# Kernel optimization log

Hardware: AMD Instinct MI355X
Metric: run time of the kernel (lower is better)

Reference implementation:

```python
import jax, jax.numpy as jnp
import numpy as np

TOKENS = 512
DIM_HEAD = 64
MAX_TOKENS = 2000
HEADS = 8
BATCH = 8


def _build_indices(tokens: int, max_tokens: int) -> np.ndarray:
    # Faithful replication of the torch index construction (done once in numpy).
    idx = np.arange(-tokens, tokens + 1)
    pad = max_tokens - 2 * tokens + 1
    row = np.concatenate([np.full(pad, idx[0]), idx, np.full(pad, idx[-1])])
    mat = np.stack([np.roll(row, i) for i in range(max_tokens)])
    mat = mat[: max_tokens - tokens + 2, max_tokens - tokens + 1 :]
    # torch fancy indexing wraps negative indices -> take mod of table size
    return (mat % (2 * tokens - 1)).astype(np.int32)


def setup_inputs() -> dict:
    key = jax.random.key(0)
    kq, kp = jax.random.split(key)
    scale = DIM_HEAD ** (-0.5)
    q = jax.random.normal(kq, (BATCH, HEADS, TOKENS, DIM_HEAD), dtype=jnp.float32)
    rel_pos_emb = (
        jax.random.normal(kp, (HEADS, 2 * TOKENS - 1, DIM_HEAD), dtype=jnp.float32)
        * scale
    )
    indices = jnp.asarray(_build_indices(TOKENS, MAX_TOKENS))
    return {"q": q, "rel_pos_emb": rel_pos_emb, "indices": indices}


def reference(q, rel_pos_emb, indices):
    t = q.shape[2]
    idx = indices[:t, :t]  # [r, t]
    # gather: [heads, r, t, dim_head]
    gathered = rel_pos_emb[:, idx]
    # emb[b,h,t,r] = sum_d q[b,h,t,d] * gathered[h,r,t,d]
    return jnp.einsum("bhtd,hrtd->bhtr", q, gathered)
```

## Files before the change

### kernel.cpp

```cpp
#include <hip/hip_runtime.h>
#include <hip/hip_bf16.h>


#define TOKENS 512
#define DIMH 64
#define NREL 1023
#define IDXN 1490

#define ESTR 72
#define PSTR 84

typedef short bf16x8 __attribute__((ext_vector_type(8)));
typedef float f32x4 __attribute__((ext_vector_type(4)));

__device__ __forceinline__ ushort4 cvt4(float4 v) {
    union { __hip_bfloat162 h2[2]; ushort4 s; } u;
    u.h2[0] = __float22bfloat162_rn(float2{v.x, v.y});
    u.h2[1] = __float22bfloat162_rn(float2{v.z, v.w});
    return u.s;
}
__device__ __forceinline__ bf16x8 cvt8(float4 a, float4 b) {
    union { __hip_bfloat162 h2[4]; bf16x8 v; } u;
    u.h2[0] = __float22bfloat162_rn(float2{a.x, a.y});
    u.h2[1] = __float22bfloat162_rn(float2{a.z, a.w});
    u.h2[2] = __float22bfloat162_rn(float2{b.x, b.y});
    u.h2[3] = __float22bfloat162_rn(float2{b.z, b.w});
    return u.v;
}

__global__ __launch_bounds__(256, 4)
void relpos_batch(const float* __restrict__ q,
                  const float* __restrict__ emb,
                  const int* __restrict__ indices,
                  float* __restrict__ out)
{
    __shared__ unsigned short Es[128 * ESTR];
    __shared__ float Ps[4 * 16 * PSTR];

    const int tid = threadIdx.x;
    const int blk = blockIdx.x;
    const int rt = blk & 7;
    const int tt = (blk >> 3) & 7;
    const int h  = (blk >> 6) & 7;
    const int bg = blk >> 9;
    const int t0 = tt * 64;
    const int r0 = rt * 64;

    const int j_a = indices[(size_t)(r0 + 63) * IDXN + t0];

    const int lane = tid & 63;
    const int wave = tid >> 6;
    const int quad = lane >> 4;
    const int l15  = lane & 15;

    {
        const float* embh = emb + (size_t)h * NREL * DIMH;
        const int c16 = tid & 15;
        const int rbase = tid >> 4;
#pragma unroll
        for (int it = 0; it < 8; ++it) {
            const int row = rbase + it * 16;
            int j = j_a + row;
            if (j >= NREL) j -= NREL;
            const float4 v = *(const float4*)(embh + (size_t)j * DIMH + c16 * 4);
            *(ushort4*)(Es + (size_t)row * ESTR + c16 * 4) = cvt4(v);
        }
    }

    const size_t qstep = (size_t)8 * TOKENS * DIMH;
    const float* qp = q + ((size_t)(bg * 32 + h) * TOKENS + t0 + wave * 16 + l15) * DIMH
                    + quad * 8;
    float4 qa0 = *(const float4*)qp;
    float4 qa1 = *(const float4*)(qp + 4);
    float4 qa2 = *(const float4*)(qp + 32);
    float4 qa3 = *(const float4*)(qp + 36);

    __syncthreads();

    bf16x8 ae[5][2];
#pragma unroll
    for (int i = 0; i < 5; ++i) {
        const unsigned short* bp = Es + (size_t)(wave * 16 + i * 16 + l15) * ESTR
                                 + quad * 8;
        ae[i][0] = *(const bf16x8*)bp;
        ae[i][1] = *(const bf16x8*)(bp + 32);
    }

    float* psw = Ps + (size_t)wave * 16 * PSTR;
    float* outw = out + ((size_t)(bg * 32 + h) * TOKENS + t0 + wave * 16) * (size_t)TOKENS
                + r0 + l15 * 4;

#pragma unroll
    for (int bi = 0; bi < 4; ++bi) {
        float4 nb0 = qa0, nb1 = qa1, nb2 = qa2, nb3 = qa3;
        if (bi < 3) {
            const float* np = qp + qstep * (bi + 1);
            nb0 = *(const float4*)np;
            nb1 = *(const float4*)(np + 4);
            nb2 = *(const float4*)(np + 32);
            nb3 = *(const float4*)(np + 36);
        }

        const bf16x8 bq0 = cvt8(qa0, qa1);
        const bf16x8 bq1 = cvt8(qa2, qa3);

#pragma unroll
        for (int i = 0; i < 5; ++i) {
            f32x4 acc = {0.f, 0.f, 0.f, 0.f};
            acc = __builtin_amdgcn_mfma_f32_16x16x32_bf16(ae[i][0], bq0, acc, 0, 0, 0);
            acc = __builtin_amdgcn_mfma_f32_16x16x32_bf16(ae[i][1], bq1, acc, 0, 0, 0);
            *(f32x4*)(psw + (size_t)l15 * PSTR + i * 16 + quad * 4) = acc;
        }

        float* ob = outw + (size_t)bi * 8 * TOKENS * TOKENS;
#pragma unroll
        for (int p = 0; p < 4; ++p) {
            const int u = quad + p * 4;
            const float* pr = psw + (size_t)u * PSTR + (u + 63 - l15 * 4);
            float4 o;
            o.x = pr[0];
            o.y = pr[-1];
            o.z = pr[-2];
            o.w = pr[-3];
            *(float4*)(ob + (size_t)u * TOKENS) = o;
        }

        qa0 = nb0; qa1 = nb1; qa2 = nb2; qa3 = nb3;
    }
}

extern "C" void kernel_launch(void* const* d_in, const int* in_sizes, int n_in,
                              void* d_out, int out_size, void* d_ws, size_t ws_size,
                              hipStream_t stream) {
    const float* q       = (const float*)d_in[0];
    const float* emb     = (const float*)d_in[1];
    const int*   indices = (const int*)d_in[2];
    float* out = (float*)d_out;

    relpos_batch<<<dim3(1024), dim3(256), 0, stream>>>(q, emb, indices, out);
}
```

Measured before the change: 98.69 us.

## Retile blocks over two r-tiles per batch with head-fastest grid and nontemporal stores

Each block now covers one batch and two 64-wide r tiles, sharing a 192-row embedding slice in LDS, instead of one r tile across four batches. The grid is reordered so the head index varies fastest, apparently to spread heads across XCDs for L2 locality, and the block count is doubled. Output writes use nontemporal stores to avoid polluting cache, and the Ps stride changes. In exchange, each block does more embedding conversion per output, loses the q prefetch overlap, and occupancy hints drop to 2.

```diff
diff --git a/kernel.cpp b/kernel.cpp
--- a/kernel.cpp
+++ b/kernel.cpp
@@ -8,7 +8,8 @@
 #define IDXN 1490
 
 #define ESTR 72
-#define PSTR 84
+#define EROWS 192
+#define PSTR 80
 
 typedef short bf16x8 __attribute__((ext_vector_type(8)));
 typedef float f32x4 __attribute__((ext_vector_type(4)));
@@ -28,25 +29,24 @@
     return u.v;
 }
 
-__global__ __launch_bounds__(256, 4)
-void relpos_batch(const float* __restrict__ q,
-                  const float* __restrict__ emb,
-                  const int* __restrict__ indices,
-                  float* __restrict__ out)
+__global__ __launch_bounds__(256, 2)
+void relpos_xcd(const float* __restrict__ q,
+                const float* __restrict__ emb,
+                const int* __restrict__ indices,
+                float* __restrict__ out)
 {
-    __shared__ unsigned short Es[128 * ESTR];
+    __shared__ unsigned short Es[EROWS * ESTR];
     __shared__ float Ps[4 * 16 * PSTR];
 
     const int tid = threadIdx.x;
     const int blk = blockIdx.x;
-    const int rt = blk & 7;
+    const int h  = blk & 7;
     const int tt = (blk >> 3) & 7;
-    const int h  = (blk >> 6) & 7;
-    const int bg = blk >> 9;
+    const int bg = (blk >> 6) & 7;
+    const int rq = blk >> 9;
     const int t0 = tt * 64;
-    const int r0 = rt * 64;
 
-    const int j_a = indices[(size_t)(r0 + 63) * IDXN + t0];
+    const int j_lo = indices[(size_t)(rq * 128 + 127) * IDXN + t0];
 
     const int lane = tid & 63;
     const int wave = tid >> 6;
@@ -56,53 +56,44 @@
     {
         const float* embh = emb + (size_t)h * NREL * DIMH;
         const int c16 = tid & 15;
-        const int rbase = tid >> 4;
+        const int r16 = tid >> 4;
 #pragma unroll
-        for (int it = 0; it < 8; ++it) {
-            const int row = rbase + it * 16;
-            int j = j_a + row;
+        for (int it = 0; it < 12; ++it) {
+            const int row = it * 16 + r16;
+            int j = j_lo + row;
             if (j >= NREL) j -= NREL;
             const float4 v = *(const float4*)(embh + (size_t)j * DIMH + c16 * 4);
             *(ushort4*)(Es + (size_t)row * ESTR + c16 * 4) = cvt4(v);
         }
     }
 
-    const size_t qstep = (size_t)8 * TOKENS * DIMH;
-    const float* qp = q + ((size_t)(bg * 32 + h) * TOKENS + t0 + wave * 16 + l15) * DIMH
-                    + quad * 8;
-    float4 qa0 = *(const float4*)qp;
-    float4 qa1 = *(const float4*)(qp + 4);
-    float4 qa2 = *(const float4*)(qp + 32);
-    float4 qa3 = *(const float4*)(qp + 36);
+    bf16x8 bq0, bq1;
+    {
+        const float* qp = q + (((size_t)bg * 8 + h) * TOKENS + t0 + wave * 16 + l15) * DIMH
+                        + quad * 8;
+        float4 a0 = *(const float4*)qp;
+        float4 a1 = *(const float4*)(qp + 4);
+        float4 b0 = *(const float4*)(qp + 32);
+        float4 b1 = *(const float4*)(qp + 36);
+        bq0 = cvt8(a0, a1);
+        bq1 = cvt8(b0, b1);
+    }
 
     __syncthreads();
 
-    bf16x8 ae[5][2];
+    float* psw = Ps + (size_t)wave * 16 * PSTR;
+
+    for (int rt = 0; rt < 2; ++rt) {
+        const int ebase = 64 * (1 - rt) + wave * 16;
+
+        bf16x8 ae[5][2];
 #pragma unroll
-    for (int i = 0; i < 5; ++i) {
-        const unsigned short* bp = Es + (size_t)(wave * 16 + i * 16 + l15) * ESTR
-                                 + quad * 8;
-        ae[i][0] = *(const bf16x8*)bp;
-        ae[i][1] = *(const bf16x8*)(bp + 32);
-    }
-
-    float* psw = Ps + (size_t)wave * 16 * PSTR;
-    float* outw = out + ((size_t)(bg * 32 + h) * TOKENS + t0 + wave * 16) * (size_t)TOKENS
-                + r0 + l15 * 4;
-
-#pragma unroll
-    for (int bi = 0; bi < 4; ++bi) {
-        float4 nb0 = qa0, nb1 = qa1, nb2 = qa2, nb3 = qa3;
-        if (bi < 3) {
-            const float* np = qp + qstep * (bi + 1);
-            nb0 = *(const float4*)np;
-            nb1 = *(const float4*)(np + 4);
-            nb2 = *(const float4*)(np + 32);
-            nb3 = *(const float4*)(np + 36);
+        for (int i = 0; i < 5; ++i) {
+            const unsigned short* ap = Es + (size_t)(ebase + i * 16 + l15) * ESTR
+                                     + quad * 8;
+            ae[i][0] = *(const bf16x8*)ap;
+            ae[i][1] = *(const bf16x8*)(ap + 32);
         }
-
-        const bf16x8 bq0 = cvt8(qa0, qa1);
-        const bf16x8 bq1 = cvt8(qa2, qa3);
 
 #pragma unroll
         for (int i = 0; i < 5; ++i) {
@@ -112,20 +103,19 @@
             *(f32x4*)(psw + (size_t)l15 * PSTR + i * 16 + quad * 4) = acc;
         }
 
-        float* ob = outw + (size_t)bi * 8 * TOKENS * TOKENS;
+        float* ob = out + (((size_t)bg * 8 + h) * TOKENS + t0 + wave * 16) * (size_t)TOKENS
+                  + rq * 128 + rt * 64 + l15 * 4;
 #pragma unroll
         for (int p = 0; p < 4; ++p) {
             const int u = quad + p * 4;
             const float* pr = psw + (size_t)u * PSTR + (u + 63 - l15 * 4);
-            float4 o;
-            o.x = pr[0];
-            o.y = pr[-1];
-            o.z = pr[-2];
-            o.w = pr[-3];
-            *(float4*)(ob + (size_t)u * TOKENS) = o;
+            f32x4 o;
+            o[0] = pr[0];
+            o[1] = pr[-1];
+            o[2] = pr[-2];
+            o[3] = pr[-3];
+            __builtin_nontemporal_store(o, (f32x4*)(ob + (size_t)u * TOKENS));
         }
-
-        qa0 = nb0; qa1 = nb1; qa2 = nb2; qa3 = nb3;
     }
 }
 
@@ -137,5 +127,5 @@
     const int*   indices = (const int*)d_in[2];
     float* out = (float*)d_out;
 
-    relpos_batch<<<dim3(1024), dim3(256), 0, stream>>>(q, emb, indices, out);
+    relpos_xcd<<<dim3(2048), dim3(256), 0, stream>>>(q, emb, indices, out);
 }
```

New measurement: 90.29 us. 8.5% less time.
